# Kernel tuning notes

Measured on AMD Instinct MI355X. Metric: run time of the kernel, lower is better.

## Reference

```python
import jax, jax.numpy as jnp
import numpy as np

N_NODES = 100000
N_EDGES = 1600000
N_GRAPHS = 256


def setup_inputs() -> dict:
    key = jax.random.key(0)
    ks = jax.random.split(key, 16)
    inp = {
        "src": jax.random.randint(ks[0], (N_EDGES,), 0, N_NODES),
        "dst": jax.random.randint(ks[1], (N_EDGES,), 0, N_NODES),
        "graph_ids": jnp.sort(jax.random.randint(ks[2], (N_NODES,), 0, N_GRAPHS)),
        "n_feat": jax.random.normal(ks[3], (N_NODES, 8), dtype=jnp.float32),
        "W1": jax.random.normal(ks[4], (8, 16), dtype=jnp.float32) * 0.25,
        "b1": jnp.zeros((16,), jnp.float32),
        "W2": jax.random.normal(ks[5], (16, 32), dtype=jnp.float32) * 0.2,
        "b2": jnp.zeros((32,), jnp.float32),
        "W3": jax.random.normal(ks[6], (32, 128), dtype=jnp.float32) * 0.15,
        "b3": jnp.zeros((128,), jnp.float32),
        "fW1": jax.random.normal(ks[7], (64, 128), dtype=jnp.float32) * 0.1,
        "fb1": jnp.zeros((128,), jnp.float32),
        "fW2": jax.random.normal(ks[8], (128, 64), dtype=jnp.float32) * 0.1,
        "fb2": jnp.zeros((64,), jnp.float32),
        "fW3": jax.random.normal(ks[9], (64, 32), dtype=jnp.float32) * 0.1,
        "fb3": jnp.zeros((32,), jnp.float32),
        "fW4": jax.random.normal(ks[10], (32, 10), dtype=jnp.float32) * 0.1,
        "fb4": jnp.zeros((10,), jnp.float32),
    }
    return inp


def reference(src, dst, graph_ids, n_feat, W1, b1, W2, b2, W3, b3,
              fW1, fb1, fW2, fb2, fW3, fb3, fW4, fb4):
    n = n_feat.shape[0]
    ones_e = jnp.ones((src.shape[0],), n_feat.dtype)
    deg_out = jax.ops.segment_sum(ones_e, src, num_segments=n)
    deg_in = jax.ops.segment_sum(ones_e, dst, num_segments=n)
    norm_out = jnp.where(deg_out > 0, deg_out ** -0.5, 0.0)  # D_out^{-1/2}
    norm_in = jnp.where(deg_in > 0, deg_in ** -0.5, 0.0)     # D_in^{-1/2}

    def gconv(x, W, b):
        # DGL GraphConv, norm='both': scale src, scatter-sum to dst, scale dst, linear
        msg = (x * norm_out[:, None])[src]           # [E, d]
        agg = jax.ops.segment_sum(msg, dst, num_segments=n)
        return (agg * norm_in[:, None]) @ W + b

    h = jax.nn.relu(gconv(n_feat, W1, b1))
    h = jax.nn.relu(gconv(h, W2, b2))
    h = gconv(h, W3, b3)                              # [N, 128]
    h = h.reshape(n, 64, 2).max(axis=-1)              # MaxPool1d(2) -> [N, 64]
    h = jax.nn.relu(h @ fW1 + fb1)
    h = jax.nn.relu(h @ fW2 + fb2)
    h = jax.nn.relu(h @ fW3 + fb3)
    h = h @ fW4 + fb4                                 # [N, 10]

    counts = jax.ops.segment_sum(jnp.ones((n,), h.dtype), graph_ids, num_segments=N_GRAPHS)
    sums = jax.ops.segment_sum(h, graph_ids, num_segments=N_GRAPHS)
    return sums / jnp.maximum(counts, 1.0)[:, None]  # dgl.mean_nodes -> [G, 10]
```

## Files before the change

### kernel.cpp

```cpp
#include <hip/hip_runtime.h>
#include <stdint.h>

#define NN 100000
#define NE 1600000
#define NG 256

#define NB 196
#define BSH 9
#define NPB 392
#define EPB 4096

typedef float f32x4 __attribute__((ext_vector_type(4)));
typedef short s16x8 __attribute__((ext_vector_type(8)));

#define WT_W3 0
#define WT_F1 4096
#define WT_F2 12288
#define WT_F3 20480
#define WT_F4 22528
#define WT_TOT 23040

#define OFF_NORM_OUT 0
#define OFF_NORM_IN  (NN)
#define OFF_INVC     (2 * NN)
#define OFF_ROWPTR   (2 * NN + 512)
#define OFF_CSR      (3 * NN + 516)
#define OFF_AGG      (3 * NN + 516 + NE)
#define OFF_BUF      (OFF_AGG + 32 * NN)
#define OFF_CNTD     (OFF_BUF + 32 * NN)
#define OFF_CNTS     (OFF_CNTD + NB * NPB)
#define OFF_BBD      (OFF_CNTS + NB * NPB)
#define OFF_BBS      (OFF_BBD + 200)
#define OFF_TOT      (OFF_BBS + 200)
#define OFF_WT       (OFF_TOT + 400)

__device__ __forceinline__ unsigned short f2bf(float f) {
  uint32_t u = __float_as_uint(f);
  u += 0x7fff + ((u >> 16) & 1);
  return (unsigned short)(u >> 16);
}
__device__ __forceinline__ float bf2f(unsigned short h) {
  return __uint_as_float(((uint32_t)h) << 16);
}

__global__ void __launch_bounds__(256) k_part_count(const int* __restrict__ src,
                                                    const int* __restrict__ dst,
                                                    int* __restrict__ cnt_dst,
                                                    int* __restrict__ cnt_src) {
  __shared__ int hd[NB], hs[NB];
  int t = threadIdx.x;
  int blk = blockIdx.x;
  for (int i = t; i < NB; i += 256) { hd[i] = 0; hs[i] = 0; }
  __syncthreads();
  int e0 = blk * EPB, e1 = min(e0 + EPB, NE);
  for (int e = e0 + t; e < e1; e += 256) {
    atomicAdd(&hd[dst[e] >> BSH], 1);
    atomicAdd(&hs[src[e] >> BSH], 1);
  }
  __syncthreads();
  for (int i = t; i < NB; i += 256) {
    cnt_dst[i * NPB + blk] = hd[i];
    cnt_src[i * NPB + blk] = hs[i];
  }
}

__global__ void __launch_bounds__(256) k_btot(const int* __restrict__ cnt_dst,
                                              const int* __restrict__ cnt_src,
                                              int* __restrict__ tot) {
  __shared__ int red[256];
  int m = blockIdx.x;
  const int* cnt = (m < NB) ? cnt_dst : cnt_src;
  int row = (m < NB) ? m : m - NB;
  int t = threadIdx.x;
  int s = 0;
  for (int k = t; k < NPB; k += 256) s += cnt[row * NPB + k];
  red[t] = s;
  __syncthreads();
  for (int off = 128; off; off >>= 1) {
    if (t < off) red[t] += red[t + off];
    __syncthreads();
  }
  if (t == 0) tot[m] = red[0];
}

__global__ void __launch_bounds__(256) k_bscan(const int* __restrict__ tot,
                                               int* __restrict__ bb_dst,
                                               int* __restrict__ bb_src) {
  __shared__ int tmp[256];
  int t = threadIdx.x;
  for (int p = 0; p < 2; ++p) {
    int* bb = p ? bb_src : bb_dst;
    int v = (t < NB) ? tot[p * NB + t] : 0;
    tmp[t] = v;
    __syncthreads();
    int incl = v;
    for (int off = 1; off < 256; off <<= 1) {
      int o = (t >= off) ? tmp[t - off] : 0;
      __syncthreads();
      incl += o;
      tmp[t] = incl;
      __syncthreads();
    }
    if (t < NB) bb[t] = incl - v;
    if (t == NB - 1) bb[NB] = incl;
    __syncthreads();
  }
}

__global__ void __launch_bounds__(256) k_crow(int* __restrict__ cnt_dst,
                                              int* __restrict__ cnt_src,
                                              const int* __restrict__ bb_dst,
                                              const int* __restrict__ bb_src) {
  __shared__ int tmp[256];
  int m = blockIdx.x;
  bool is_src = m >= NB;
  int row = is_src ? m - NB : m;
  int* cnt = is_src ? cnt_src : cnt_dst;
  const int* bb = is_src ? bb_src : bb_dst;
  int t = threadIdx.x;
  int i0 = 2 * t, i1 = 2 * t + 1;
  int v0 = (i0 < NPB) ? cnt[row * NPB + i0] : 0;
  int v1 = (i1 < NPB) ? cnt[row * NPB + i1] : 0;
  int ps = v0 + v1;
  tmp[t] = ps;
  __syncthreads();
  int incl = ps;
  for (int off = 1; off < 256; off <<= 1) {
    int o = (t >= off) ? tmp[t - off] : 0;
    __syncthreads();
    incl += o;
    tmp[t] = incl;
    __syncthreads();
  }
  int ex = incl - ps + bb[row];
  if (i0 < NPB) cnt[row * NPB + i0] = ex;
  if (i1 < NPB) cnt[row * NPB + i1] = ex + v0;
}

__global__ void __launch_bounds__(256) k_part_scatter(const int* __restrict__ src,
                                                      const int* __restrict__ dst,
                                                      const int* __restrict__ cnt_dst,
                                                      const int* __restrict__ cnt_src,
                                                      uint32_t* __restrict__ pairs,
                                                      uint16_t* __restrict__ srcbuf) {
  __shared__ int cd[NB], cs[NB];
  int t = threadIdx.x;
  int blk = blockIdx.x;
  for (int i = t; i < NB; i += 256) {
    cd[i] = cnt_dst[i * NPB + blk];
    cs[i] = cnt_src[i * NPB + blk];
  }
  __syncthreads();
  int e0 = blk * EPB, e1 = min(e0 + EPB, NE);
  for (int e = e0 + t; e < e1; e += 256) {
    int s = src[e], d = dst[e];
    int pd = atomicAdd(&cd[d >> BSH], 1);
    pairs[pd] = ((uint32_t)s << 9) | (uint32_t)(d & 511);
    int ps = atomicAdd(&cs[s >> BSH], 1);
    srcbuf[ps] = (uint16_t)(s & 511);
  }
}

__global__ void __launch_bounds__(256) k_bucket_csr(const uint32_t* __restrict__ pairs,
                                                    const int* __restrict__ bb,
                                                    int* __restrict__ row_ptr,
                                                    float* __restrict__ norm_in,
                                                    int* __restrict__ csr) {
  __shared__ int hist[512], curs[512], pscan[256];
  int t = threadIdx.x;
  int b = blockIdx.x;
  int n0 = b << BSH;
  int ebase = bb[b], eend = bb[b + 1];
  hist[t] = 0;
  hist[t + 256] = 0;
  __syncthreads();
  for (int e = ebase + t; e < eend; e += 256)
    atomicAdd(&hist[pairs[e] & 511], 1);
  __syncthreads();
  int s0 = hist[2 * t], s1 = hist[2 * t + 1];
  int ps = s0 + s1;
  pscan[t] = ps;
  __syncthreads();
  int incl = ps;
  for (int off = 1; off < 256; off <<= 1) {
    int o = (t >= off) ? pscan[t - off] : 0;
    __syncthreads();
    incl += o;
    pscan[t] = incl;
    __syncthreads();
  }
  int ex = incl - ps;
  curs[2 * t] = ex;
  curs[2 * t + 1] = ex + s0;
  int n = n0 + 2 * t;
  if (n < NN) {
    row_ptr[n] = ebase + ex;
    norm_in[n] = s0 > 0 ? 1.0f / sqrtf((float)s0) : 0.0f;
  }
  if (n + 1 < NN) {
    row_ptr[n + 1] = ebase + ex + s0;
    norm_in[n + 1] = s1 > 0 ? 1.0f / sqrtf((float)s1) : 0.0f;
  }
  __syncthreads();
  for (int e = ebase + t; e < eend; e += 256) {
    uint32_t pr = pairs[e];
    int pos = atomicAdd(&curs[pr & 511], 1);
    csr[ebase + pos] = (int)(pr >> 9);
  }
  if (b == 0 && t == 0) row_ptr[NN] = NE;
}

__global__ void __launch_bounds__(256) k_bucket_deg(const uint16_t* __restrict__ srcbuf,
                                                    const int* __restrict__ bb,
                                                    const float* __restrict__ n_feat,
                                                    float* __restrict__ norm_out,
                                                    unsigned short* __restrict__ xsb) {
  __shared__ int hist[512];
  int t = threadIdx.x;
  int b = blockIdx.x;
  hist[t] = 0;
  hist[t + 256] = 0;
  __syncthreads();
  int e0 = bb[b], e1 = bb[b + 1];
  for (int e = e0 + t; e < e1; e += 256)
    atomicAdd(&hist[srcbuf[e]], 1);
  __syncthreads();
#pragma unroll
  for (int h = 0; h < 2; ++h) {
    int n = (b << BSH) + t + h * 256;
    if (n < NN) {
      int d = hist[t + h * 256];
      float no = d > 0 ? 1.0f / sqrtf((float)d) : 0.0f;
      norm_out[n] = no;
      float4 a = *reinterpret_cast<const float4*>(n_feat + (size_t)n * 8);
      float4 bb4 = *reinterpret_cast<const float4*>(n_feat + (size_t)n * 8 + 4);
      s16x8 o;
      o[0] = (short)f2bf(a.x * no);   o[1] = (short)f2bf(a.y * no);
      o[2] = (short)f2bf(a.z * no);   o[3] = (short)f2bf(a.w * no);
      o[4] = (short)f2bf(bb4.x * no); o[5] = (short)f2bf(bb4.y * no);
      o[6] = (short)f2bf(bb4.z * no); o[7] = (short)f2bf(bb4.w * no);
      *reinterpret_cast<s16x8*>(&xsb[(size_t)n * 8]) = o;
    }
  }
}

__global__ void __launch_bounds__(NG) k_graphinfo(const int* __restrict__ gid,
                                                  float* __restrict__ inv) {
  int g = threadIdx.x;
  int lo0 = 0, hi0 = NN;
  while (lo0 < hi0) { int m = (lo0 + hi0) >> 1; if (gid[m] < g) lo0 = m + 1; else hi0 = m; }
  int lo1 = lo0, hi1 = NN;
  while (lo1 < hi1) { int m = (lo1 + hi1) >> 1; if (gid[m] < g + 1) lo1 = m + 1; else hi1 = m; }
  int c = lo1 - lo0;
  inv[g] = 1.0f / fmaxf((float)c, 1.0f);
}

template <int DIN, int DOUT>
__global__ void __launch_bounds__(256) k_agglayer(
    const unsigned short* __restrict__ xs, const int* __restrict__ csr,
    const int* __restrict__ row_ptr, const float* __restrict__ norm_in,
    const float* __restrict__ norm_out, const float* __restrict__ W,
    const float* __restrict__ bvec, unsigned short* __restrict__ ys) {
  int i = blockIdx.x * 256 + threadIdx.x;
  if (i >= NN) return;
  float acc[DIN];
#pragma unroll
  for (int k = 0; k < DIN; ++k) acc[k] = 0.f;
  int e0 = row_ptr[i], e1 = row_ptr[i + 1];
  for (int e = e0; e < e1; ++e) {
    int s = csr[e];
#pragma unroll
    for (int c = 0; c < DIN / 8; ++c) {
      s16x8 v = *reinterpret_cast<const s16x8*>(&xs[(size_t)s * DIN + c * 8]);
#pragma unroll
      for (int j = 0; j < 8; ++j)
        acc[c * 8 + j] += bf2f((unsigned short)v[j]);
    }
  }
  float ni = norm_in[i];
#pragma unroll
  for (int k = 0; k < DIN; ++k) acc[k] *= ni;
  float no = norm_out[i];
  float y[DOUT];
#pragma unroll
  for (int j = 0; j < DOUT; ++j) {
    float s = bvec[j];
#pragma unroll
    for (int k = 0; k < DIN; ++k) s = fmaf(acc[k], W[k * DOUT + j], s);
    y[j] = fmaxf(s, 0.f) * no;
  }
#pragma unroll
  for (int c = 0; c < DOUT / 8; ++c) {
    s16x8 o;
#pragma unroll
    for (int j = 0; j < 8; ++j) o[j] = (short)f2bf(y[c * 8 + j]);
    *reinterpret_cast<s16x8*>(&ys[(size_t)i * DOUT + c * 8]) = o;
  }
}

__global__ void k_agg32_bf(const unsigned short* __restrict__ xs,
                           const int* __restrict__ csr,
                           const int* __restrict__ row_ptr,
                           const float* __restrict__ norm_in,
                           unsigned short* __restrict__ aggb) {
  int t = blockIdx.x * blockDim.x + threadIdx.x;
  if (t >= NN * 4) return;
  int i = t >> 2;
  int c = t & 3;
  int e0 = row_ptr[i], e1 = row_ptr[i + 1];
  float acc[8];
#pragma unroll
  for (int j = 0; j < 8; ++j) acc[j] = 0.f;
  for (int e = e0; e < e1; ++e) {
    int s = csr[e];
    s16x8 v = *reinterpret_cast<const s16x8*>(&xs[(size_t)s * 32 + c * 8]);
#pragma unroll
    for (int j = 0; j < 8; ++j) acc[j] += bf2f((unsigned short)v[j]);
  }
  float ni = norm_in[i];
  s16x8 o;
#pragma unroll
  for (int j = 0; j < 8; ++j) o[j] = (short)f2bf(acc[j] * ni);
  *reinterpret_cast<s16x8*>(&aggb[(size_t)i * 32 + c * 8]) = o;
}

__global__ void __launch_bounds__(256) k_prepw(
    const float* __restrict__ W3, const float* __restrict__ fW1,
    const float* __restrict__ fW2, const float* __restrict__ fW3,
    const float* __restrict__ fW4, unsigned short* __restrict__ wT,
    float* __restrict__ out, int out_size) {
  int t = threadIdx.x;
  for (int i = t; i < out_size; i += 256) out[i] = 0.f;
  for (int i = t; i < 4096; i += 256) {
    int n = i >> 5, k = i & 31;
    wT[WT_W3 + ((n * 32 + k) ^ ((n & 3) << 3))] = f2bf(W3[k * 128 + n]);
  }
  for (int i = t; i < 8192; i += 256) {
    int n = i >> 6, k = i & 63;
    wT[WT_F1 + ((n * 64 + k) ^ ((n & 7) << 3))] = f2bf(fW1[k * 128 + n]);
  }
  for (int i = t; i < 8192; i += 256) {
    int n = i >> 7, k = i & 127;
    wT[WT_F2 + ((n * 128 + k) ^ ((n & 7) << 3))] = f2bf(fW2[k * 64 + n]);
  }
  for (int i = t; i < 2048; i += 256) {
    int n = i >> 6, k = i & 63;
    wT[WT_F3 + ((n * 64 + k) ^ ((n & 7) << 3))] = f2bf(fW3[k * 32 + n]);
  }
  for (int i = t; i < 512; i += 256) {
    int n = i >> 5, k = i & 31;
    float v = (n < 10) ? fW4[k * 10 + n] : 0.f;
    wT[WT_F4 + ((n * 32 + k) ^ ((n & 3) << 3))] = f2bf(v);
  }
}

__global__ void __launch_bounds__(256) k_tail9(
    const unsigned short* __restrict__ aggb, const int* __restrict__ gid,
    const unsigned short* __restrict__ wT,
    const float* __restrict__ b3, const float* __restrict__ fb1,
    const float* __restrict__ fb2, const float* __restrict__ fb3,
    const float* __restrict__ fb4, const float* __restrict__ inv_counts,
    float* __restrict__ out) {
  __shared__ __align__(16) unsigned short wv[WT_TOT];
  __shared__ __align__(16) unsigned short acts[4 * 3072];
  __shared__ int sgid[256];
  int t = threadIdx.x;
  int l = t & 63;
  int w = t >> 6;
  int nb = blockIdx.x * 256;

  for (int i = t; i < WT_TOT / 8; i += 256)
    *reinterpret_cast<s16x8*>(&wv[i * 8]) =
        *reinterpret_cast<const s16x8*>(&wT[i * 8]);
  if (nb + t < NN) sgid[t] = gid[nb + t]; else sgid[t] = 0x7fffffff;
  __syncthreads();

  unsigned short* bufA = acts + w * 3072;
  unsigned short* bufB = acts + w * 3072 + 2048;
  int m = l & 15;
  int kg = l >> 4;
  float fc4r[16];

#pragma unroll
  for (int g = 0; g < 4; ++g) {
    int base = nb + w * 64 + g * 16;
    {
      int n16 = l >> 2, kq = l & 3;
      int node = base + n16;
      s16x8 xpk = {0, 0, 0, 0, 0, 0, 0, 0};
      if (node < NN)
        xpk = *reinterpret_cast<const s16x8*>(&aggb[(size_t)node * 32 + kq * 8]);
      int e = (n16 * 64 + kq * 8) ^ ((n16 & 7) << 3);
      *reinterpret_cast<s16x8*>(&bufA[e]) = xpk;
    }
    asm volatile("s_waitcnt lgkmcnt(0)" ::: "memory");

#pragma unroll
    for (int nt = 0; nt < 8; ++nt) {
      int n = nt * 16 + m;
      f32x4 acc = {0.f, 0.f, 0.f, 0.f};
      s16x8 a = *reinterpret_cast<const s16x8*>(
          &bufA[(m * 64 + kg * 8) ^ ((m & 7) << 3)]);
      s16x8 b = *reinterpret_cast<const s16x8*>(
          &wv[WT_W3 + ((n * 32 + kg * 8) ^ ((n & 3) << 3))]);
      acc = __builtin_amdgcn_mfma_f32_16x16x32_bf16(a, b, acc, 0, 0, 0);
      float bias = b3[n];
#pragma unroll
      for (int r = 0; r < 4; ++r) {
        float v = acc[r] + bias;
        float pv = fmaxf(v, __shfl_xor(v, 1));
        if (!(m & 1)) {
          int node = kg * 4 + r;
          int j = n >> 1;
          bufB[(node * 64 + j) ^ ((node & 7) << 3)] = f2bf(pv);
        }
      }
    }
    asm volatile("s_waitcnt lgkmcnt(0)" ::: "memory");
#pragma unroll
    for (int nt = 0; nt < 8; ++nt) {
      int n = nt * 16 + m;
      f32x4 acc = {0.f, 0.f, 0.f, 0.f};
#pragma unroll
      for (int kt = 0; kt < 2; ++kt) {
        s16x8 a = *reinterpret_cast<const s16x8*>(
            &bufB[(m * 64 + kt * 32 + kg * 8) ^ ((m & 7) << 3)]);
        s16x8 b = *reinterpret_cast<const s16x8*>(
            &wv[WT_F1 + ((n * 64 + kt * 32 + kg * 8) ^ ((n & 7) << 3))]);
        acc = __builtin_amdgcn_mfma_f32_16x16x32_bf16(a, b, acc, 0, 0, 0);
      }
      float bias = fb1[n];
#pragma unroll
      for (int r = 0; r < 4; ++r) {
        int node = kg * 4 + r;
        float v = fmaxf(acc[r] + bias, 0.f);
        bufA[(node * 128 + n) ^ ((node & 7) << 3)] = f2bf(v);
      }
    }
    asm volatile("s_waitcnt lgkmcnt(0)" ::: "memory");
#pragma unroll
    for (int nt = 0; nt < 4; ++nt) {
      int n = nt * 16 + m;
      f32x4 acc = {0.f, 0.f, 0.f, 0.f};
#pragma unroll
      for (int kt = 0; kt < 4; ++kt) {
        s16x8 a = *reinterpret_cast<const s16x8*>(
            &bufA[(m * 128 + kt * 32 + kg * 8) ^ ((m & 7) << 3)]);
        s16x8 b = *reinterpret_cast<const s16x8*>(
            &wv[WT_F2 + ((n * 128 + kt * 32 + kg * 8) ^ ((n & 7) << 3))]);
        acc = __builtin_amdgcn_mfma_f32_16x16x32_bf16(a, b, acc, 0, 0, 0);
      }
      float bias = fb2[n];
#pragma unroll
      for (int r = 0; r < 4; ++r) {
        int node = kg * 4 + r;
        float v = fmaxf(acc[r] + bias, 0.f);
        bufB[(node * 64 + n) ^ ((node & 7) << 3)] = f2bf(v);
      }
    }
    asm volatile("s_waitcnt lgkmcnt(0)" ::: "memory");
#pragma unroll
    for (int nt = 0; nt < 2; ++nt) {
      int n = nt * 16 + m;
      f32x4 acc = {0.f, 0.f, 0.f, 0.f};
#pragma unroll
      for (int kt = 0; kt < 2; ++kt) {
        s16x8 a = *reinterpret_cast<const s16x8*>(
            &bufB[(m * 64 + kt * 32 + kg * 8) ^ ((m & 7) << 3)]);
        s16x8 b = *reinterpret_cast<const s16x8*>(
            &wv[WT_F3 + ((n * 64 + kt * 32 + kg * 8) ^ ((n & 7) << 3))]);
        acc = __builtin_amdgcn_mfma_f32_16x16x32_bf16(a, b, acc, 0, 0, 0);
      }
      float bias = fb3[n];
#pragma unroll
      for (int r = 0; r < 4; ++r) {
        int node = kg * 4 + r;
        float v = fmaxf(acc[r] + bias, 0.f);
        bufA[(node * 64 + n) ^ ((node & 7) << 3)] = f2bf(v);
      }
    }
    asm volatile("s_waitcnt lgkmcnt(0)" ::: "memory");
    {
      f32x4 acc = {0.f, 0.f, 0.f, 0.f};
      s16x8 a = *reinterpret_cast<const s16x8*>(
          &bufA[(m * 64 + kg * 8) ^ ((m & 7) << 3)]);
      s16x8 b = *reinterpret_cast<const s16x8*>(
          &wv[WT_F4 + ((m * 32 + kg * 8) ^ ((m & 3) << 3))]);
      acc = __builtin_amdgcn_mfma_f32_16x16x32_bf16(a, b, acc, 0, 0, 0);
      float bias = (m < 10) ? fb4[m] : 0.f;
#pragma unroll
      for (int r = 0; r < 4; ++r) fc4r[g * 4 + r] = acc[r] + bias;
    }
  }

  asm volatile("s_waitcnt lgkmcnt(0)" ::: "memory");
  {
    float* fbuf = reinterpret_cast<float*>(bufA);
    if (m < 10) {
#pragma unroll
      for (int g = 0; g < 4; ++g)
#pragma unroll
        for (int r = 0; r < 4; ++r) {
          int nl = g * 16 + kg * 4 + r;
          fbuf[nl * 12 + m] = fc4r[g * 4 + r];
        }
    }
  }
  __syncthreads();

  if (t < 40) {
    int q = t / 10, j = t % 10;
    const float* fbuf = reinterpret_cast<const float*>(acts + q * 3072);
    int qbase = q * 64;
    int qrem = min(64, NN - (nb + qbase));
    if (qrem > 0) {
      int g = sgid[qbase];
      float run = 0.f;
      for (int n = 0; n < qrem; ++n) {
        run += fbuf[n * 12 + j];
        bool last = (n == qrem - 1) || (sgid[qbase + n + 1] != g);
        if (last) {
          atomicAdd(&out[g * 10 + j], run * inv_counts[g]);
          run = 0.f;
          if (n < qrem - 1) g = sgid[qbase + n + 1];
        }
      }
    }
  }
}

extern "C" void kernel_launch(void* const* d_in, const int* in_sizes, int n_in,
                              void* d_out, int out_size, void* d_ws, size_t ws_size,
                              hipStream_t stream) {
  const int* src = (const int*)d_in[0];
  const int* dst = (const int*)d_in[1];
  const int* gid = (const int*)d_in[2];
  const float* n_feat = (const float*)d_in[3];
  const float* W1 = (const float*)d_in[4];
  const float* b1 = (const float*)d_in[5];
  const float* W2 = (const float*)d_in[6];
  const float* b2 = (const float*)d_in[7];
  const float* W3 = (const float*)d_in[8];
  const float* b3 = (const float*)d_in[9];
  const float* fW1 = (const float*)d_in[10];
  const float* fb1 = (const float*)d_in[11];
  const float* fW2 = (const float*)d_in[12];
  const float* fb2 = (const float*)d_in[13];
  const float* fW3 = (const float*)d_in[14];
  const float* fb3 = (const float*)d_in[15];
  const float* fW4 = (const float*)d_in[16];
  const float* fb4 = (const float*)d_in[17];
  float* out = (float*)d_out;

  float* ws = (float*)d_ws;
  float* norm_out = ws + OFF_NORM_OUT;
  float* norm_in = ws + OFF_NORM_IN;
  float* inv_cnt = ws + OFF_INVC;
  int* row_ptr = (int*)(ws + OFF_ROWPTR);
  int* csr = (int*)(ws + OFF_CSR);
  float* agg = ws + OFF_AGG;
  float* buf = ws + OFF_BUF;
  int* cnt_dst = (int*)(ws + OFF_CNTD);
  int* cnt_src = (int*)(ws + OFF_CNTS);
  int* bb_dst = (int*)(ws + OFF_BBD);
  int* bb_src = (int*)(ws + OFF_BBS);
  int* tot = (int*)(ws + OFF_TOT);
  unsigned short* wT = (unsigned short*)(ws + OFF_WT);
  uint32_t* pairs = (uint32_t*)agg;
  uint16_t* srcbuf = (uint16_t*)((int*)agg + NE);
  unsigned short* xs0b = (unsigned short*)buf;
  unsigned short* xs1b = (unsigned short*)agg;
  unsigned short* xs2b = (unsigned short*)buf;
  unsigned short* aggb = (unsigned short*)agg;

  k_prepw<<<1, 256, 0, stream>>>(W3, fW1, fW2, fW3, fW4, wT, out, out_size);
  k_part_count<<<NPB, 256, 0, stream>>>(src, dst, cnt_dst, cnt_src);
  k_graphinfo<<<1, NG, 0, stream>>>(gid, inv_cnt);
  k_btot<<<2 * NB, 256, 0, stream>>>(cnt_dst, cnt_src, tot);
  k_bscan<<<1, 256, 0, stream>>>(tot, bb_dst, bb_src);
  k_crow<<<2 * NB, 256, 0, stream>>>(cnt_dst, cnt_src, bb_dst, bb_src);
  k_part_scatter<<<NPB, 256, 0, stream>>>(src, dst, cnt_dst, cnt_src, pairs, srcbuf);
  k_bucket_csr<<<NB, 256, 0, stream>>>(pairs, bb_dst, row_ptr, norm_in, csr);
  k_bucket_deg<<<NB, 256, 0, stream>>>(srcbuf, bb_src, n_feat, norm_out, xs0b);

  k_agglayer<8, 16><<<(NN + 255) / 256, 256, 0, stream>>>(
      xs0b, csr, row_ptr, norm_in, norm_out, W1, b1, xs1b);
  k_agglayer<16, 32><<<(NN + 255) / 256, 256, 0, stream>>>(
      xs1b, csr, row_ptr, norm_in, norm_out, W2, b2, xs2b);
  k_agg32_bf<<<(NN * 4 + 255) / 256, 256, 0, stream>>>(xs2b, csr, row_ptr, norm_in, aggb);
  k_tail9<<<(NN + 255) / 256, 256, 0, stream>>>(aggb, gid, wT, b3, fb1, fb2, fb3, fb4,
                                                inv_cnt, out);
}
```

Before: 216.0 us.

## Merge preprocessing kernels to cut launch count and serial small launches

Folds the graph-count binary search into the weight-prep kernel, has every k_crow block redundantly scan the bucket totals (which removes the single-block k_bscan), and merges the dst CSR bucket and src degree kernels into one 2*NB-block launch. The goal is to remove three kernel launches, the serialization they force, and the idle GPU time spent in tiny single-block kernels. In exchange each k_crow block repeats a 256-wide scan, and the merged bucket kernel has two unevenly sized halves whose shared-memory use is set by the larger branch.

After: 202.1 us. 6.4% less time.

```diff
diff --git a/kernel.cpp b/kernel.cpp
--- a/kernel.cpp
+++ b/kernel.cpp
@@ -43,6 +43,46 @@
   return __uint_as_float(((uint32_t)h) << 16);
 }
 
+__global__ void __launch_bounds__(256) k_prepw(
+    const float* __restrict__ W3, const float* __restrict__ fW1,
+    const float* __restrict__ fW2, const float* __restrict__ fW3,
+    const float* __restrict__ fW4, unsigned short* __restrict__ wT,
+    float* __restrict__ out, int out_size,
+    const int* __restrict__ gid, float* __restrict__ inv) {
+  int t = threadIdx.x;
+  for (int i = t; i < out_size; i += 256) out[i] = 0.f;
+  for (int i = t; i < 4096; i += 256) {
+    int n = i >> 5, k = i & 31;
+    wT[WT_W3 + ((n * 32 + k) ^ ((n & 3) << 3))] = f2bf(W3[k * 128 + n]);
+  }
+  for (int i = t; i < 8192; i += 256) {
+    int n = i >> 6, k = i & 63;
+    wT[WT_F1 + ((n * 64 + k) ^ ((n & 7) << 3))] = f2bf(fW1[k * 128 + n]);
+  }
+  for (int i = t; i < 8192; i += 256) {
+    int n = i >> 7, k = i & 127;
+    wT[WT_F2 + ((n * 128 + k) ^ ((n & 7) << 3))] = f2bf(fW2[k * 64 + n]);
+  }
+  for (int i = t; i < 2048; i += 256) {
+    int n = i >> 6, k = i & 63;
+    wT[WT_F3 + ((n * 64 + k) ^ ((n & 7) << 3))] = f2bf(fW3[k * 32 + n]);
+  }
+  for (int i = t; i < 512; i += 256) {
+    int n = i >> 5, k = i & 31;
+    float v = (n < 10) ? fW4[k * 10 + n] : 0.f;
+    wT[WT_F4 + ((n * 32 + k) ^ ((n & 3) << 3))] = f2bf(v);
+  }
+  {
+    int g = t;
+    int lo0 = 0, hi0 = NN;
+    while (lo0 < hi0) { int m = (lo0 + hi0) >> 1; if (gid[m] < g) lo0 = m + 1; else hi0 = m; }
+    int lo1 = lo0, hi1 = NN;
+    while (lo1 < hi1) { int m = (lo1 + hi1) >> 1; if (gid[m] < g + 1) lo1 = m + 1; else hi1 = m; }
+    int c = lo1 - lo0;
+    inv[g] = 1.0f / fmaxf((float)c, 1.0f);
+  }
+}
+
 __global__ void __launch_bounds__(256) k_part_count(const int* __restrict__ src,
                                                     const int* __restrict__ dst,
                                                     int* __restrict__ cnt_dst,
@@ -83,56 +123,55 @@
   if (t == 0) tot[m] = red[0];
 }
 
-__global__ void __launch_bounds__(256) k_bscan(const int* __restrict__ tot,
-                                               int* __restrict__ bb_dst,
-                                               int* __restrict__ bb_src) {
-  __shared__ int tmp[256];
-  int t = threadIdx.x;
-  for (int p = 0; p < 2; ++p) {
-    int* bb = p ? bb_src : bb_dst;
-    int v = (t < NB) ? tot[p * NB + t] : 0;
-    tmp[t] = v;
-    __syncthreads();
-    int incl = v;
-    for (int off = 1; off < 256; off <<= 1) {
-      int o = (t >= off) ? tmp[t - off] : 0;
-      __syncthreads();
-      incl += o;
-      tmp[t] = incl;
-      __syncthreads();
-    }
-    if (t < NB) bb[t] = incl - v;
-    if (t == NB - 1) bb[NB] = incl;
-    __syncthreads();
-  }
-}
-
 __global__ void __launch_bounds__(256) k_crow(int* __restrict__ cnt_dst,
                                               int* __restrict__ cnt_src,
-                                              const int* __restrict__ bb_dst,
-                                              const int* __restrict__ bb_src) {
+                                              const int* __restrict__ tot,
+                                              int* __restrict__ bb_dst,
+                                              int* __restrict__ bb_src) {
   __shared__ int tmp[256];
+  __shared__ int sbase;
   int m = blockIdx.x;
   bool is_src = m >= NB;
   int row = is_src ? m - NB : m;
   int* cnt = is_src ? cnt_src : cnt_dst;
-  const int* bb = is_src ? bb_src : bb_dst;
-  int t = threadIdx.x;
+  int* bb = is_src ? bb_src : bb_dst;
+  const int* trow = tot + (is_src ? NB : 0);
+  int t = threadIdx.x;
+
+  int v = (t < NB) ? trow[t] : 0;
+  tmp[t] = v;
+  __syncthreads();
+  int incl = v;
+  for (int off = 1; off < 256; off <<= 1) {
+    int o = (t >= off) ? tmp[t - off] : 0;
+    __syncthreads();
+    incl += o;
+    tmp[t] = incl;
+    __syncthreads();
+  }
+  if (t == row) sbase = incl - v;
+  if (row == 0) {
+    if (t < NB) bb[t] = incl - v;
+    if (t == NB - 1) bb[NB] = incl;
+  }
+  __syncthreads();
+  int base = sbase;
+
   int i0 = 2 * t, i1 = 2 * t + 1;
   int v0 = (i0 < NPB) ? cnt[row * NPB + i0] : 0;
   int v1 = (i1 < NPB) ? cnt[row * NPB + i1] : 0;
   int ps = v0 + v1;
   tmp[t] = ps;
   __syncthreads();
-  int incl = ps;
+  int incl2 = ps;
   for (int off = 1; off < 256; off <<= 1) {
     int o = (t >= off) ? tmp[t - off] : 0;
     __syncthreads();
-    incl += o;
-    tmp[t] = incl;
-    __syncthreads();
-  }
-  int ex = incl - ps + bb[row];
+    incl2 += o;
+    tmp[t] = incl2;
+    __syncthreads();
+  }
+  int ex = incl2 - ps + base;
   if (i0 < NPB) cnt[row * NPB + i0] = ex;
   if (i1 < NPB) cnt[row * NPB + i1] = ex + v0;
 }
@@ -161,98 +200,83 @@
   }
 }
 
-__global__ void __launch_bounds__(256) k_bucket_csr(const uint32_t* __restrict__ pairs,
-                                                    const int* __restrict__ bb,
-                                                    int* __restrict__ row_ptr,
-                                                    float* __restrict__ norm_in,
-                                                    int* __restrict__ csr) {
+__global__ void __launch_bounds__(256) k_bucket(
+    const uint32_t* __restrict__ pairs, const int* __restrict__ bb_dst,
+    const uint16_t* __restrict__ srcbuf, const int* __restrict__ bb_src,
+    const float* __restrict__ n_feat,
+    int* __restrict__ row_ptr, float* __restrict__ norm_in, int* __restrict__ csr,
+    float* __restrict__ norm_out, unsigned short* __restrict__ xsb) {
   __shared__ int hist[512], curs[512], pscan[256];
   int t = threadIdx.x;
-  int b = blockIdx.x;
-  int n0 = b << BSH;
-  int ebase = bb[b], eend = bb[b + 1];
-  hist[t] = 0;
-  hist[t + 256] = 0;
-  __syncthreads();
-  for (int e = ebase + t; e < eend; e += 256)
-    atomicAdd(&hist[pairs[e] & 511], 1);
-  __syncthreads();
-  int s0 = hist[2 * t], s1 = hist[2 * t + 1];
-  int ps = s0 + s1;
-  pscan[t] = ps;
-  __syncthreads();
-  int incl = ps;
-  for (int off = 1; off < 256; off <<= 1) {
-    int o = (t >= off) ? pscan[t - off] : 0;
-    __syncthreads();
-    incl += o;
-    pscan[t] = incl;
-    __syncthreads();
-  }
-  int ex = incl - ps;
-  curs[2 * t] = ex;
-  curs[2 * t + 1] = ex + s0;
-  int n = n0 + 2 * t;
-  if (n < NN) {
-    row_ptr[n] = ebase + ex;
-    norm_in[n] = s0 > 0 ? 1.0f / sqrtf((float)s0) : 0.0f;
-  }
-  if (n + 1 < NN) {
-    row_ptr[n + 1] = ebase + ex + s0;
-    norm_in[n + 1] = s1 > 0 ? 1.0f / sqrtf((float)s1) : 0.0f;
-  }
-  __syncthreads();
-  for (int e = ebase + t; e < eend; e += 256) {
-    uint32_t pr = pairs[e];
-    int pos = atomicAdd(&curs[pr & 511], 1);
-    csr[ebase + pos] = (int)(pr >> 9);
-  }
-  if (b == 0 && t == 0) row_ptr[NN] = NE;
-}
-
-__global__ void __launch_bounds__(256) k_bucket_deg(const uint16_t* __restrict__ srcbuf,
-                                                    const int* __restrict__ bb,
-                                                    const float* __restrict__ n_feat,
-                                                    float* __restrict__ norm_out,
-                                                    unsigned short* __restrict__ xsb) {
-  __shared__ int hist[512];
-  int t = threadIdx.x;
-  int b = blockIdx.x;
-  hist[t] = 0;
-  hist[t + 256] = 0;
-  __syncthreads();
-  int e0 = bb[b], e1 = bb[b + 1];
-  for (int e = e0 + t; e < e1; e += 256)
-    atomicAdd(&hist[srcbuf[e]], 1);
-  __syncthreads();
-#pragma unroll
-  for (int h = 0; h < 2; ++h) {
-    int n = (b << BSH) + t + h * 256;
+  int m = blockIdx.x;
+  if (m < NB) {
+    int b = m;
+    int n0 = b << BSH;
+    int ebase = bb_dst[b], eend = bb_dst[b + 1];
+    hist[t] = 0;
+    hist[t + 256] = 0;
+    __syncthreads();
+    for (int e = ebase + t; e < eend; e += 256)
+      atomicAdd(&hist[pairs[e] & 511], 1);
+    __syncthreads();
+    int s0 = hist[2 * t], s1 = hist[2 * t + 1];
+    int ps = s0 + s1;
+    pscan[t] = ps;
+    __syncthreads();
+    int incl = ps;
+    for (int off = 1; off < 256; off <<= 1) {
+      int o = (t >= off) ? pscan[t - off] : 0;
+      __syncthreads();
+      incl += o;
+      pscan[t] = incl;
+      __syncthreads();
+    }
+    int ex = incl - ps;
+    curs[2 * t] = ex;
+    curs[2 * t + 1] = ex + s0;
+    int n = n0 + 2 * t;
     if (n < NN) {
-      int d = hist[t + h * 256];
-      float no = d > 0 ? 1.0f / sqrtf((float)d) : 0.0f;
-      norm_out[n] = no;
-      float4 a = *reinterpret_cast<const float4*>(n_feat + (size_t)n * 8);
-      float4 bb4 = *reinterpret_cast<const float4*>(n_feat + (size_t)n * 8 + 4);
-      s16x8 o;
-      o[0] = (short)f2bf(a.x * no);   o[1] = (short)f2bf(a.y * no);
-      o[2] = (short)f2bf(a.z * no);   o[3] = (short)f2bf(a.w * no);
-      o[4] = (short)f2bf(bb4.x * no); o[5] = (short)f2bf(bb4.y * no);
-      o[6] = (short)f2bf(bb4.z * no); o[7] = (short)f2bf(bb4.w * no);
-      *reinterpret_cast<s16x8*>(&xsb[(size_t)n * 8]) = o;
-    }
-  }
-}
-
-__global__ void __launch_bounds__(NG) k_graphinfo(const int* __restrict__ gid,
-                                                  float* __restrict__ inv) {
-  int g = threadIdx.x;
-  int lo0 = 0, hi0 = NN;
-  while (lo0 < hi0) { int m = (lo0 + hi0) >> 1; if (gid[m] < g) lo0 = m + 1; else hi0 = m; }
-  int lo1 = lo0, hi1 = NN;
-  while (lo1 < hi1) { int m = (lo1 + hi1) >> 1; if (gid[m] < g + 1) lo1 = m + 1; else hi1 = m; }
-  int c = lo1 - lo0;
-  inv[g] = 1.0f / fmaxf((float)c, 1.0f);
+      row_ptr[n] = ebase + ex;
+      norm_in[n] = s0 > 0 ? 1.0f / sqrtf((float)s0) : 0.0f;
+    }
+    if (n + 1 < NN) {
+      row_ptr[n + 1] = ebase + ex + s0;
+      norm_in[n + 1] = s1 > 0 ? 1.0f / sqrtf((float)s1) : 0.0f;
+    }
+    __syncthreads();
+    for (int e = ebase + t; e < eend; e += 256) {
+      uint32_t pr = pairs[e];
+      int pos = atomicAdd(&curs[pr & 511], 1);
+      csr[ebase + pos] = (int)(pr >> 9);
+    }
+    if (b == 0 && t == 0) row_ptr[NN] = NE;
+  } else {
+    int b = m - NB;
+    hist[t] = 0;
+    hist[t + 256] = 0;
+    __syncthreads();
+    int e0 = bb_src[b], e1 = bb_src[b + 1];
+    for (int e = e0 + t; e < e1; e += 256)
+      atomicAdd(&hist[srcbuf[e]], 1);
+    __syncthreads();
+#pragma unroll
+    for (int h = 0; h < 2; ++h) {
+      int n = (b << BSH) + t + h * 256;
+      if (n < NN) {
+        int d = hist[t + h * 256];
+        float no = d > 0 ? 1.0f / sqrtf((float)d) : 0.0f;
+        norm_out[n] = no;
+        float4 a = *reinterpret_cast<const float4*>(n_feat + (size_t)n * 8);
+        float4 bb4 = *reinterpret_cast<const float4*>(n_feat + (size_t)n * 8 + 4);
+        s16x8 o;
+        o[0] = (short)f2bf(a.x * no);   o[1] = (short)f2bf(a.y * no);
+        o[2] = (short)f2bf(a.z * no);   o[3] = (short)f2bf(a.w * no);
+        o[4] = (short)f2bf(bb4.x * no); o[5] = (short)f2bf(bb4.y * no);
+        o[6] = (short)f2bf(bb4.z * no); o[7] = (short)f2bf(bb4.w * no);
+        *reinterpret_cast<s16x8*>(&xsb[(size_t)n * 8]) = o;
+      }
+    }
+  }
 }
 
 template <int DIN, int DOUT>
@@ -322,36 +346,6 @@
 #pragma unroll
   for (int j = 0; j < 8; ++j) o[j] = (short)f2bf(acc[j] * ni);
   *reinterpret_cast<s16x8*>(&aggb[(size_t)i * 32 + c * 8]) = o;
-}
-
-__global__ void __launch_bounds__(256) k_prepw(
-    const float* __restrict__ W3, const float* __restrict__ fW1,
-    const float* __restrict__ fW2, const float* __restrict__ fW3,
-    const float* __restrict__ fW4, unsigned short* __restrict__ wT,
-    float* __restrict__ out, int out_size) {
-  int t = threadIdx.x;
-  for (int i = t; i < out_size; i += 256) out[i] = 0.f;
-  for (int i = t; i < 4096; i += 256) {
-    int n = i >> 5, k = i & 31;
-    wT[WT_W3 + ((n * 32 + k) ^ ((n & 3) << 3))] = f2bf(W3[k * 128 + n]);
-  }
-  for (int i = t; i < 8192; i += 256) {
-    int n = i >> 6, k = i & 63;
-    wT[WT_F1 + ((n * 64 + k) ^ ((n & 7) << 3))] = f2bf(fW1[k * 128 + n]);
-  }
-  for (int i = t; i < 8192; i += 256) {
-    int n = i >> 7, k = i & 127;
-    wT[WT_F2 + ((n * 128 + k) ^ ((n & 7) << 3))] = f2bf(fW2[k * 64 + n]);
-  }
-  for (int i = t; i < 2048; i += 256) {
-    int n = i >> 6, k = i & 63;
-    wT[WT_F3 + ((n * 64 + k) ^ ((n & 7) << 3))] = f2bf(fW3[k * 32 + n]);
-  }
-  for (int i = t; i < 512; i += 256) {
-    int n = i >> 5, k = i & 31;
-    float v = (n < 10) ? fW4[k * 10 + n] : 0.f;
-    wT[WT_F4 + ((n * 32 + k) ^ ((n & 3) << 3))] = f2bf(v);
-  }
 }
 
 __global__ void __launch_bounds__(256) k_tail9(
@@ -573,15 +567,13 @@
   unsigned short* xs2b = (unsigned short*)buf;
   unsigned short* aggb = (unsigned short*)agg;
 
-  k_prepw<<<1, 256, 0, stream>>>(W3, fW1, fW2, fW3, fW4, wT, out, out_size);
+  k_prepw<<<1, 256, 0, stream>>>(W3, fW1, fW2, fW3, fW4, wT, out, out_size, gid, inv_cnt);
   k_part_count<<<NPB, 256, 0, stream>>>(src, dst, cnt_dst, cnt_src);
-  k_graphinfo<<<1, NG, 0, stream>>>(gid, inv_cnt);
   k_btot<<<2 * NB, 256, 0, stream>>>(cnt_dst, cnt_src, tot);
-  k_bscan<<<1, 256, 0, stream>>>(tot, bb_dst, bb_src);
-  k_crow<<<2 * NB, 256, 0, stream>>>(cnt_dst, cnt_src, bb_dst, bb_src);
+  k_crow<<<2 * NB, 256, 0, stream>>>(cnt_dst, cnt_src, tot, bb_dst, bb_src);
   k_part_scatter<<<NPB, 256, 0, stream>>>(src, dst, cnt_dst, cnt_src, pairs, srcbuf);
-  k_bucket_csr<<<NB, 256, 0, stream>>>(pairs, bb_dst, row_ptr, norm_in, csr);
-  k_bucket_deg<<<NB, 256, 0, stream>>>(srcbuf, bb_src, n_feat, norm_out, xs0b);
+  k_bucket<<<2 * NB, 256, 0, stream>>>(pairs, bb_dst, srcbuf, bb_src, n_feat,
+                                       row_ptr, norm_in, csr, norm_out, xs0b);
 
   k_agglayer<8, 16><<<(NN + 255) / 256, 256, 0, stream>>>(
       xs0b, csr, row_ptr, norm_in, norm_out, W1, b1, xs1b);
```
